# Optimization experiments

Measured on AMD Instinct MI355X. Metric: run time of the kernel, lower is better.

## Reference

```python
import jax, jax.numpy as jnp
import numpy as np
import math

B, L, M = 8, 1024, 1024
H, D, DK, DFF = 16, 1024, 64, 4096
EPS = 1e-5


def _ln(x, g, b):
    mu = jnp.mean(x, axis=-1, keepdims=True)
    var = jnp.mean((x - mu) ** 2, axis=-1, keepdims=True)
    return (x - mu) * jax.lax.rsqrt(var + EPS) * g + b


def _mha(x, kv, Wq, bq, Wk, bk, Wv, bv, Wo, bo, masked):
    # x: [B,Lq,D], kv: [B,Lk,D]; per-head weights stacked: Wq [H,D,DK], bq [H,DK]
    Q = jnp.einsum('bld,hdk->bhlk', x, Wq) + bq[None, :, None, :]
    K = jnp.einsum('bld,hdk->bhlk', kv, Wk) + bk[None, :, None, :]
    V = jnp.einsum('bld,hdk->bhlk', kv, Wv) + bv[None, :, None, :]
    scores = jnp.einsum('bhqk,bhmk->bhqm', Q, K) / math.sqrt(DK)
    p = jax.nn.softmax(scores, axis=-1)
    if masked:
        # faithful to source: mask applied AFTER softmax (multiply by tril ones)
        Lq = x.shape[1]
        tril = jnp.tril(jnp.ones((Lq, kv.shape[1]), dtype=p.dtype))
        p = p * tril
    z = jnp.einsum('bhqm,bhmk->bhqk', p, V)  # [B,H,Lq,DK]
    z = jnp.transpose(z, (0, 2, 1, 3)).reshape(x.shape[0], x.shape[1], H * DK)
    return z @ Wo + bo


def _forward(x, enc, Wq1, bq1, Wk1, bk1, Wv1, bv1, Wo1, bo1,
             Wq2, bq2, Wk2, bk2, Wv2, bv2, Wo2, bo2,
             W1, b1, W2, b2, g1, be1, g2, be2, g3, be3):
    z = _mha(x, x, Wq1, bq1, Wk1, bk1, Wv1, bv1, Wo1, bo1, masked=True)
    x = _ln(z + x, g1, be1)
    z = _mha(x, enc, Wq2, bq2, Wk2, bk2, Wv2, bv2, Wo2, bo2, masked=False)
    x = _ln(z + x, g2, be2)
    # Conv1d(k=1) pair == per-token MLP: relu(x @ W1 + b1) @ W2 + b2
    y = jax.nn.relu(x @ W1 + b1) @ W2 + b2
    return _ln(y + x, g3, be3)


def setup_inputs() -> dict:
    key = jax.random.key(0)
    ks = jax.random.split(key, 16)
    s = 0.02
    return {
        'x': jax.random.normal(ks[0], (B, L, D), jnp.float32),
        'enc': jax.random.normal(ks[1], (B, M, D), jnp.float32),
        'Wq1': jax.random.normal(ks[2], (H, D, DK), jnp.float32) * s,
        'bq1': jnp.zeros((H, DK), jnp.float32),
        'Wk1': jax.random.normal(ks[3], (H, D, DK), jnp.float32) * s,
        'bk1': jnp.zeros((H, DK), jnp.float32),
        'Wv1': jax.random.normal(ks[4], (H, D, DK), jnp.float32) * s,
        'bv1': jnp.zeros((H, DK), jnp.float32),
        'Wo1': jax.random.normal(ks[5], (H * DK, D), jnp.float32) * s,
        'bo1': jnp.zeros((D,), jnp.float32),
        'Wq2': jax.random.normal(ks[6], (H, D, DK), jnp.float32) * s,
        'bq2': jnp.zeros((H, DK), jnp.float32),
        'Wk2': jax.random.normal(ks[7], (H, D, DK), jnp.float32) * s,
        'bk2': jnp.zeros((H, DK), jnp.float32),
        'Wv2': jax.random.normal(ks[8], (H, D, DK), jnp.float32) * s,
        'bv2': jnp.zeros((H, DK), jnp.float32),
        'Wo2': jax.random.normal(ks[9], (H * DK, D), jnp.float32) * s,
        'bo2': jnp.zeros((D,), jnp.float32),
        'W1': jax.random.normal(ks[10], (D, DFF), jnp.float32) * s,
        'b1': jnp.zeros((DFF,), jnp.float32),
        'W2': jax.random.normal(ks[11], (DFF, D), jnp.float32) * s,
        'b2': jnp.zeros((D,), jnp.float32),
        'g1': jnp.ones((D,), jnp.float32), 'be1': jnp.zeros((D,), jnp.float32),
        'g2': jnp.ones((D,), jnp.float32), 'be2': jnp.zeros((D,), jnp.float32),
        'g3': jnp.ones((D,), jnp.float32), 'be3': jnp.zeros((D,), jnp.float32),
    }


def reference(x, enc, Wq1, bq1, Wk1, bk1, Wv1, bv1, Wo1, bo1,
              Wq2, bq2, Wk2, bk2, Wv2, bv2, Wo2, bo2,
              W1, b1, W2, b2, g1, be1, g2, be2, g3, be3):
    return _forward(x, enc, Wq1, bq1, Wk1, bk1, Wv1, bv1, Wo1, bo1,
                    Wq2, bq2, Wk2, bk2, Wv2, bv2, Wo2, bo2,
                    W1, b1, W2, b2, g1, be1, g2, be2, g3, be3)
```

## Files before the change

### kernel.cpp

```cpp
#include <hip/hip_runtime.h>
#include <hip/hip_bf16.h>

typedef __bf16 bf16;
typedef __bf16 bf16x8 __attribute__((ext_vector_type(8)));
typedef __bf16 bf16x4v __attribute__((ext_vector_type(4)));
typedef float f32x4 __attribute__((ext_vector_type(4)));
typedef unsigned int u32;
typedef u32 u32x4 __attribute__((ext_vector_type(4)));

#define DEV static __device__ __forceinline__

DEV void gll16(const void* g, void* l) {
  __builtin_amdgcn_global_load_lds((__attribute__((address_space(1))) void*)g,
                                   (__attribute__((address_space(3))) void*)l,
                                   16, 0, 0);
}

DEV bf16 tobf(float f) { return (bf16)f; }

DEV u32 cvtpk(float lo, float hi) {
  u32 r;
  asm("v_cvt_pk_bf16_f32 %0, %1, %2" : "=v"(r) : "v"(lo), "v"(hi));
  return r;
}

__global__ void cast_f2b_kernel(const float* __restrict__ in, bf16* __restrict__ out, int n4) {
  int i = blockIdx.x * 256 + threadIdx.x;
  if (i < n4) {
    const float4 v = ((const float4*)in)[i];
    bf16x4v o;
    o[0] = tobf(v.x); o[1] = tobf(v.y); o[2] = tobf(v.z); o[3] = tobf(v.w);
    ((bf16x4v*)out)[i] = o;
  }
}

__global__ __launch_bounds__(256)
void tpack_kernel(const float* __restrict__ in, bf16* __restrict__ out,
                  int K, int N, int in_hs, int out_hs, float scale) {
  __shared__ float tile[32][33];
  const int k0 = blockIdx.x << 5, n0 = blockIdx.y << 5;
  const float* ip = in + (size_t)blockIdx.z * in_hs;
  bf16* op = out + (size_t)blockIdx.z * out_hs;
  const int tx = threadIdx.x & 31, ty = threadIdx.x >> 5;
#pragma unroll
  for (int r = 0; r < 4; ++r)
    tile[ty * 4 + r][tx] = ip[(size_t)(k0 + ty * 4 + r) * N + n0 + tx];
  __syncthreads();
#pragma unroll
  for (int r = 0; r < 4; ++r)
    op[(size_t)(n0 + ty * 4 + r) * K + k0 + tx] = tobf(tile[tx][ty * 4 + r] * scale);
}

__global__ void bscale_kernel(const float* __restrict__ in, float* __restrict__ out, int n, float s) {
  int i = blockIdx.x * 256 + threadIdx.x;
  if (i < n) out[i] = in[i] * s;
}

template<int EPI>
__global__ __launch_bounds__(256, 2)
void gemm_bt(const bf16* __restrict__ A, const bf16* __restrict__ W,
             const float* __restrict__ bias, const float* __restrict__ resid,
             void* __restrict__ outv, int M, int N, int K) {
  __shared__ bf16 sA[2][128 * 64];
  __shared__ bf16 sB[2][128 * 64];
  const int nbx = N >> 7;
  const int nwg = (M >> 7) * nbx;
  int bid = (int)blockIdx.x;
  bid = (bid & 7) * (nwg >> 3) + (bid >> 3);
  const int tm = bid / nbx, tn = bid - tm * nbx;
  const int tid = threadIdx.x;
  const int lane = tid & 63;
  const int w = tid >> 6;
  const int wm = (w >> 1) << 6, wn = (w & 1) << 6;
  const int l15 = lane & 15, l4 = lane >> 4;

  int srow[4], scol[4];
#pragma unroll
  for (int j = 0; j < 4; ++j) {
    int g = tid + (j << 8);
    srow[j] = g >> 3;
    scol[j] = ((g & 7) ^ (srow[j] & 7)) << 3;
  }
  const bf16* Abase = A + (size_t)(tm * 128) * K;
  const bf16* Bbase = W + (size_t)(tn * 128) * K;

  f32x4 acc[4][4] = {};
  const int nt = K >> 6;
  int cur = 0;

  auto stage = [&](int buf, int t) {
    const int kb = t << 6;
#pragma unroll
    for (int j = 0; j < 4; ++j) {
      int g = tid + (j << 8);
      gll16(Abase + (size_t)srow[j] * K + kb + scol[j], &sA[buf][g << 3]);
    }
#pragma unroll
    for (int j = 0; j < 4; ++j) {
      int g = tid + (j << 8);
      gll16(Bbase + (size_t)srow[j] * K + kb + scol[j], &sB[buf][g << 3]);
    }
  };

  stage(0, 0);
  __syncthreads();

  for (int t = 0; t < nt; ++t) {
    if (t + 1 < nt) stage(cur ^ 1, t + 1);
    bf16x8 af[4][2], bfm[4][2];
#pragma unroll
    for (int mi = 0; mi < 4; ++mi)
#pragma unroll
      for (int kk = 0; kk < 2; ++kk) {
        int r = wm + (mi << 4) + l15;
        int off = (r << 7) + (kk << 6) + (l4 << 4);
        off ^= (r & 7) << 4;
        af[mi][kk] = *(const bf16x8*)((const char*)sA[cur] + off);
      }
#pragma unroll
    for (int ni = 0; ni < 4; ++ni)
#pragma unroll
      for (int kk = 0; kk < 2; ++kk) {
        int r = wn + (ni << 4) + l15;
        int off = (r << 7) + (kk << 6) + (l4 << 4);
        off ^= (r & 7) << 4;
        bfm[ni][kk] = *(const bf16x8*)((const char*)sB[cur] + off);
      }
#pragma unroll
    for (int mi = 0; mi < 4; ++mi)
#pragma unroll
      for (int ni = 0; ni < 4; ++ni)
#pragma unroll
        for (int kk = 0; kk < 2; ++kk)
          acc[mi][ni] = __builtin_amdgcn_mfma_f32_16x16x32_bf16(af[mi][kk], bfm[ni][kk],
                                                                acc[mi][ni], 0, 0, 0);
    __syncthreads();
    cur ^= 1;
  }

  const int row0 = tm * 128 + wm + (l4 << 2);
  const int col0 = tn * 128 + wn + l15;
#pragma unroll
  for (int ni = 0; ni < 4; ++ni) {
    const int col = col0 + (ni << 4);
    const float bv = bias ? bias[col] : 0.f;
#pragma unroll
    for (int mi = 0; mi < 4; ++mi) {
      const int rr = row0 + (mi << 4);
      f32x4 v = acc[mi][ni];
      if (EPI == 0) {
        bf16* out = (bf16*)outv;
#pragma unroll
        for (int r = 0; r < 4; ++r) out[(size_t)(rr + r) * N + col] = tobf(v[r] + bv);
      } else if (EPI == 1) {
        float* out = (float*)outv;
#pragma unroll
        for (int r = 0; r < 4; ++r) {
          size_t idx = (size_t)(rr + r) * N + col;
          out[idx] = v[r] + bv + resid[idx];
        }
      } else if (EPI == 2) {
        bf16* out = (bf16*)outv;
#pragma unroll
        for (int r = 0; r < 4; ++r) out[(size_t)(rr + r) * N + col] = tobf(fmaxf(v[r] + bv, 0.f));
      } else {
        bf16* out = (bf16*)outv;
        const int bb = rr >> 10, l0 = rr & 1023;
        const int hh = col >> 6, dk = col & 63;
        bf16x4v pk;
#pragma unroll
        for (int r = 0; r < 4; ++r) pk[r] = tobf(v[r] + bv);
        *(bf16x4v*)(out + ((size_t)((bb * 16 + hh) * 64 + dk) << 10) + l0) = pk;
      }
    }
  }
}

template<bool MASKED>
__global__ __launch_bounds__(256, 4)
void attn_kernel(const bf16* __restrict__ Qp, const bf16* __restrict__ Kp,
                 const bf16* __restrict__ Vt, bf16* __restrict__ Z) {
  __shared__ bf16 sK[2][64 * 64];
  __shared__ bf16 sV[2][64 * 64];
  const int Lk = 1024;
  const int d = blockIdx.x;
  const int bh = d & 127, qb = d >> 7;
  const int b = bh >> 4, h = bh & 15;
  const int q0 = qb << 7;
  const int tid = threadIdx.x, lane = tid & 63, w = tid >> 6;
  const int l15 = lane & 15, l4 = lane >> 4;

  const bf16* Qb = Qp + ((size_t)(b * 1024 + q0 + w * 32)) * 1024 + h * 64;
  bf16x8 qf[2][2];
#pragma unroll
  for (int mi = 0; mi < 2; ++mi)
#pragma unroll
    for (int kk = 0; kk < 2; ++kk)
      qf[mi][kk] = *(const bf16x8*)(Qb + (size_t)((mi << 4) + l15) * 1024 + (kk << 5) + (l4 << 3));

  f32x4 o[4][2] = {};
  float Mr[2] = {-1e30f, -1e30f}, Lr[2] = {0.f, 0.f};

  const bf16* Kb = Kp + ((size_t)b * Lk) * 1024 + h * 64;
  const bf16* Vb = Vt + ((size_t)(b * 16 + h)) * 64 * Lk;

  auto stage = [&](int buf, int t, bool withV) {
    const int kv0 = t << 6;
#pragma unroll
    for (int j = 0; j < 2; ++j) {
      int g = tid + (j << 8);
      int r = g >> 3;
      int sc = ((g & 7) ^ (r & 7)) << 3;
      gll16(Kb + (size_t)(kv0 + r) * 1024 + sc, &sK[buf][g << 3]);
      if (withV) gll16(Vb + (size_t)r * Lk + kv0 + sc, &sV[buf][g << 3]);
    }
  };
  auto needPV = [&](int t) -> bool { return !MASKED || ((t << 6) < q0 + 128); };

  const int NT = Lk >> 6;
  stage(0, 0, true);
  __syncthreads();
  int cur = 0;

  for (int t = 0; t < NT; ++t) {
    if (t + 1 < NT) stage(cur ^ 1, t + 1, needPV(t + 1));
    const int kv0 = t << 6;

    f32x4 s[4][2] = {};
#pragma unroll
    for (int n = 0; n < 4; ++n) {
      bf16x8 kf[2];
#pragma unroll
      for (int kk = 0; kk < 2; ++kk) {
        int r = (n << 4) + l15;
        int off = (r << 7) + (kk << 6) + (l4 << 4);
        off ^= (r & 7) << 4;
        kf[kk] = *(const bf16x8*)((const char*)sK[cur] + off);
      }
#pragma unroll
      for (int mi = 0; mi < 2; ++mi)
#pragma unroll
        for (int kk = 0; kk < 2; ++kk)
          s[n][mi] = __builtin_amdgcn_mfma_f32_16x16x32_bf16(kf[kk], qf[mi][kk],
                                                             s[n][mi], 0, 0, 0);
    }

    float alv[2];
#pragma unroll
    for (int mi = 0; mi < 2; ++mi) {
      float tmx = s[0][mi][0];
#pragma unroll
      for (int n = 0; n < 4; ++n)
#pragma unroll
        for (int r = 0; r < 4; ++r) tmx = fmaxf(tmx, s[n][mi][r]);
      tmx = fmaxf(tmx, __shfl_xor(tmx, 16, 64));
      tmx = fmaxf(tmx, __shfl_xor(tmx, 32, 64));
      const float Mn = fmaxf(Mr[mi], tmx);
      alv[mi] = exp2f(Mr[mi] - Mn);
      float rs = 0.f;
#pragma unroll
      for (int n = 0; n < 4; ++n)
#pragma unroll
        for (int r = 0; r < 4; ++r) {
          float p = exp2f(s[n][mi][r] - Mn);
          s[n][mi][r] = p;
          rs += p;
        }
      rs += __shfl_xor(rs, 16, 64);
      rs += __shfl_xor(rs, 32, 64);
      Lr[mi] = Lr[mi] * alv[mi] + rs;
      Mr[mi] = Mn;
    }

#pragma unroll
    for (int mi = 0; mi < 2; ++mi)
#pragma unroll
      for (int r = 0; r < 4; ++r) {
        float a = __shfl(alv[mi], (l4 << 2) + r, 64);
#pragma unroll
        for (int nd = 0; nd < 4; ++nd) o[nd][mi][r] *= a;
      }

    if (needPV(t)) {
      const bool needMask = MASKED && (kv0 + 63 > q0 + (w << 5));
      bf16x8 pa[2][2];
#pragma unroll
      for (int mi = 0; mi < 2; ++mi) {
        u32 D0[4], D1[4];
        const int qg = q0 + (w << 5) + (mi << 4) + l15;
#pragma unroll
        for (int n = 0; n < 4; ++n) {
          float pv[4];
#pragma unroll
          for (int r = 0; r < 4; ++r) {
            float p = s[n][mi][r];
            if (needMask) {
              int cg = kv0 + (n << 4) + (l4 << 2) + r;
              if (cg > qg) p = 0.f;
            }
            pv[r] = p;
          }
          D0[n] = cvtpk(pv[0], pv[1]);
          D1[n] = cvtpk(pv[2], pv[3]);
        }
        const int src = l15 + ((lane & 16) << 1);
#pragma unroll
        for (int kk = 0; kk < 2; ++kk) {
          u32 v0 = (lane & 32) ? D0[2 * kk + 1] : D0[2 * kk];
          u32 v1 = (lane & 32) ? D1[2 * kk + 1] : D1[2 * kk];
          u32x4 tw;
          tw[0] = (u32)__shfl((int)v0, src, 64);
          tw[1] = (u32)__shfl((int)v1, src, 64);
          tw[2] = (u32)__shfl((int)v0, src + 16, 64);
          tw[3] = (u32)__shfl((int)v1, src + 16, 64);
          pa[mi][kk] = *(bf16x8*)&tw;
        }
      }
#pragma unroll
      for (int nd = 0; nd < 4; ++nd) {
        bf16x8 vf[2];
#pragma unroll
        for (int kk = 0; kk < 2; ++kk) {
          int r = (nd << 4) + l15;
          int off = (r << 7) + (kk << 6) + (l4 << 4);
          off ^= (r & 7) << 4;
          vf[kk] = *(const bf16x8*)((const char*)sV[cur] + off);
        }
#pragma unroll
        for (int mi = 0; mi < 2; ++mi)
#pragma unroll
          for (int kk = 0; kk < 2; ++kk)
            o[nd][mi] = __builtin_amdgcn_mfma_f32_16x16x32_bf16(pa[mi][kk], vf[kk],
                                                                o[nd][mi], 0, 0, 0);
      }
    }
    __syncthreads();
    cur ^= 1;
  }

  float inv[2][4];
#pragma unroll
  for (int mi = 0; mi < 2; ++mi) {
    float il = 1.f / Lr[mi];
#pragma unroll
    for (int r = 0; r < 4; ++r) inv[mi][r] = __shfl(il, (l4 << 2) + r, 64);
  }
  bf16* Zb = Z + ((size_t)(b * 1024 + q0 + w * 32)) * 1024 + h * 64;
#pragma unroll
  for (int nd = 0; nd < 4; ++nd)
#pragma unroll
    for (int mi = 0; mi < 2; ++mi)
#pragma unroll
      for (int r = 0; r < 4; ++r)
        Zb[(size_t)((mi << 4) + (l4 << 2) + r) * 1024 + (nd << 4) + l15] =
            tobf(o[nd][mi][r] * inv[mi][r]);
}

__global__ __launch_bounds__(256)
void ln_kernel(const float* __restrict__ in, const float* __restrict__ gw,
               const float* __restrict__ bw, float* __restrict__ outf,
               bf16* __restrict__ outb) {
  const int row = blockIdx.x, tid = threadIdx.x;
  const size_t base = (size_t)row << 10;
  const float4 v = *(const float4*)(in + base + tid * 4);
  float s = v.x + v.y + v.z + v.w;
  float ss = v.x * v.x + v.y * v.y + v.z * v.z + v.w * v.w;
#pragma unroll
  for (int d = 1; d < 64; d <<= 1) { s += __shfl_xor(s, d, 64); ss += __shfl_xor(ss, d, 64); }
  __shared__ float red[8];
  const int w = tid >> 6;
  if ((tid & 63) == 0) { red[w] = s; red[4 + w] = ss; }
  __syncthreads();
  s = red[0] + red[1] + red[2] + red[3];
  ss = red[4] + red[5] + red[6] + red[7];
  const float mu = s * (1.f / 1024.f);
  const float var = ss * (1.f / 1024.f) - mu * mu;
  const float rstd = rsqrtf(var + 1e-5f);
  const float4 g4 = *(const float4*)(gw + tid * 4);
  const float4 b4 = *(const float4*)(bw + tid * 4);
  const float o0 = (v.x - mu) * rstd * g4.x + b4.x;
  const float o1 = (v.y - mu) * rstd * g4.y + b4.y;
  const float o2 = (v.z - mu) * rstd * g4.z + b4.z;
  const float o3 = (v.w - mu) * rstd * g4.w + b4.w;
  if (outf) { float4 of; of.x = o0; of.y = o1; of.z = o2; of.w = o3;
              *(float4*)(outf + base + tid * 4) = of; }
  if (outb) { bf16x4v ob; ob[0] = tobf(o0); ob[1] = tobf(o1); ob[2] = tobf(o2); ob[3] = tobf(o3);
              *(bf16x4v*)(outb + base + tid * 4) = ob; }
}

extern "C" void kernel_launch(void* const* d_in, const int* in_sizes, int n_in,
                              void* d_out, int out_size, void* d_ws, size_t ws_size,
                              hipStream_t stream) {
  const float* x   = (const float*)d_in[0];
  const float* enc = (const float*)d_in[1];
  const float* Wq1 = (const float*)d_in[2];
  const float* bq1 = (const float*)d_in[3];
  const float* Wk1 = (const float*)d_in[4];
  const float* bk1 = (const float*)d_in[5];
  const float* Wv1 = (const float*)d_in[6];
  const float* bv1 = (const float*)d_in[7];
  const float* Wo1 = (const float*)d_in[8];
  const float* bo1 = (const float*)d_in[9];
  const float* Wq2 = (const float*)d_in[10];
  const float* bq2 = (const float*)d_in[11];
  const float* Wk2 = (const float*)d_in[12];
  const float* bk2 = (const float*)d_in[13];
  const float* Wv2 = (const float*)d_in[14];
  const float* bv2 = (const float*)d_in[15];
  const float* Wo2 = (const float*)d_in[16];
  const float* bo2 = (const float*)d_in[17];
  const float* W1  = (const float*)d_in[18];
  const float* b1  = (const float*)d_in[19];
  const float* W2  = (const float*)d_in[20];
  const float* b2  = (const float*)d_in[21];
  const float* g1  = (const float*)d_in[22];
  const float* be1 = (const float*)d_in[23];
  const float* g2  = (const float*)d_in[24];
  const float* be2 = (const float*)d_in[25];
  const float* g3  = (const float*)d_in[26];
  const float* be3 = (const float*)d_in[27];

  char* ws = (char*)d_ws;
  size_t off = 0;
  auto alloc = [&](size_t bytes) { char* p = ws + off; off += (bytes + 255) & ~(size_t)255; return p; };
  const size_t ACT = (size_t)8 * 1024 * 1024 * 2;
  const size_t WSQ = (size_t)1024 * 1024 * 2;
  const float QSC = 0.125f * 1.44269504088896f;

  bf16* xb    = (bf16*)alloc(ACT);
  bf16* encb  = (bf16*)alloc(ACT);
  bf16* Wq1t  = (bf16*)alloc(WSQ);
  bf16* Wk1t  = (bf16*)alloc(WSQ);
  bf16* Wv1t  = (bf16*)alloc(WSQ);
  bf16* Wq2t  = (bf16*)alloc(WSQ);
  bf16* Wk2t  = (bf16*)alloc(WSQ);
  bf16* Wv2t  = (bf16*)alloc(WSQ);
  bf16* Wo1t  = (bf16*)alloc(WSQ);
  bf16* Wo2t  = (bf16*)alloc(WSQ);
  bf16* W1t   = (bf16*)alloc((size_t)4096 * 1024 * 2);
  bf16* W2t   = (bf16*)alloc((size_t)4096 * 1024 * 2);
  float* sbq1 = (float*)alloc(4096);
  float* sbq2 = (float*)alloc(4096);
  char*  S    = alloc((size_t)64 * 1024 * 1024);
  float* rbuf = (float*)alloc((size_t)8 * 1024 * 1024 * 4);
  float* xnf  = (float*)alloc((size_t)8 * 1024 * 1024 * 4);
  bf16*  xnb  = (bf16*)alloc(ACT);

  bf16* q1   = (bf16*)(S);
  bf16* k1   = (bf16*)(S + ACT);
  bf16* vt1  = (bf16*)(S + 2 * ACT);
  bf16* z1   = (bf16*)(S + 3 * ACT);
  bf16* hbuf = (bf16*)S;

  dim3 b256(256);
  cast_f2b_kernel<<<8192, b256, 0, stream>>>(x, xb, 2097152);
  cast_f2b_kernel<<<8192, b256, 0, stream>>>(enc, encb, 2097152);
  tpack_kernel<<<dim3(32, 2, 16), b256, 0, stream>>>(Wq1, Wq1t, 1024, 64, 65536, 65536, QSC);
  tpack_kernel<<<dim3(32, 2, 16), b256, 0, stream>>>(Wk1, Wk1t, 1024, 64, 65536, 65536, 1.f);
  tpack_kernel<<<dim3(32, 2, 16), b256, 0, stream>>>(Wv1, Wv1t, 1024, 64, 65536, 65536, 1.f);
  tpack_kernel<<<dim3(32, 2, 16), b256, 0, stream>>>(Wq2, Wq2t, 1024, 64, 65536, 65536, QSC);
  tpack_kernel<<<dim3(32, 2, 16), b256, 0, stream>>>(Wk2, Wk2t, 1024, 64, 65536, 65536, 1.f);
  tpack_kernel<<<dim3(32, 2, 16), b256, 0, stream>>>(Wv2, Wv2t, 1024, 64, 65536, 65536, 1.f);
  tpack_kernel<<<dim3(32, 32, 1), b256, 0, stream>>>(Wo1, Wo1t, 1024, 1024, 0, 0, 1.f);
  tpack_kernel<<<dim3(32, 32, 1), b256, 0, stream>>>(Wo2, Wo2t, 1024, 1024, 0, 0, 1.f);
  tpack_kernel<<<dim3(32, 128, 1), b256, 0, stream>>>(W1, W1t, 1024, 4096, 0, 0, 1.f);
  tpack_kernel<<<dim3(128, 32, 1), b256, 0, stream>>>(W2, W2t, 4096, 1024, 0, 0, 1.f);
  bscale_kernel<<<4, b256, 0, stream>>>(bq1, sbq1, 1024, QSC);
  bscale_kernel<<<4, b256, 0, stream>>>(bq2, sbq2, 1024, QSC);

  gemm_bt<0><<<512, b256, 0, stream>>>(xb, Wq1t, sbq1, nullptr, q1, 8192, 1024, 1024);
  gemm_bt<0><<<512, b256, 0, stream>>>(xb, Wk1t, bk1, nullptr, k1, 8192, 1024, 1024);
  gemm_bt<3><<<512, b256, 0, stream>>>(xb, Wv1t, bv1, nullptr, vt1, 8192, 1024, 1024);
  attn_kernel<true><<<1024, b256, 0, stream>>>(q1, k1, vt1, z1);
  gemm_bt<1><<<512, b256, 0, stream>>>(z1, Wo1t, bo1, x, rbuf, 8192, 1024, 1024);
  ln_kernel<<<8192, b256, 0, stream>>>(rbuf, g1, be1, xnf, xnb);

  gemm_bt<0><<<512, b256, 0, stream>>>(xnb, Wq2t, sbq2, nullptr, q1, 8192, 1024, 1024);
  gemm_bt<0><<<512, b256, 0, stream>>>(encb, Wk2t, bk2, nullptr, k1, 8192, 1024, 1024);
  gemm_bt<3><<<512, b256, 0, stream>>>(encb, Wv2t, bv2, nullptr, vt1, 8192, 1024, 1024);
  attn_kernel<false><<<1024, b256, 0, stream>>>(q1, k1, vt1, z1);
  gemm_bt<1><<<512, b256, 0, stream>>>(z1, Wo2t, bo2, xnf, rbuf, 8192, 1024, 1024);
  ln_kernel<<<8192, b256, 0, stream>>>(rbuf, g2, be2, xnf, xnb);

  gemm_bt<2><<<2048, b256, 0, stream>>>(xnb, W1t, b1, nullptr, hbuf, 8192, 4096, 1024);
  gemm_bt<1><<<512, b256, 0, stream>>>(hbuf, W2t, b2, xnf, rbuf, 8192, 1024, 4096);
  ln_kernel<<<8192, b256, 0, stream>>>(rbuf, g3, be3, (float*)d_out, nullptr);
}
```

Before: 693.9 us.

## Fuse QKV and KV projection GEMMs into single wide GEMM launches

Packs the Q/K/V weights (and cross-attention K/V weights) into one concatenated weight matrix and runs a single GEMM with N=3072 or 2048 instead of three or two separate launches. A new epilogue routes each column segment to Q/K row-major output or transposed V output. This saves launch overhead and tail effects, and gives each launch more blocks to fill the GPU. It also lowers the attention kernel's occupancy hint from 4 to 3 waves-per-block launch bound, which frees registers at the cost of fewer resident blocks.

```diff
diff --git a/kernel.cpp b/kernel.cpp
--- a/kernel.cpp
+++ b/kernel.cpp
@@ -163,7 +163,7 @@
         bf16* out = (bf16*)outv;
 #pragma unroll
         for (int r = 0; r < 4; ++r) out[(size_t)(rr + r) * N + col] = tobf(fmaxf(v[r] + bv, 0.f));
-      } else {
+      } else if (EPI == 3) {
         bf16* out = (bf16*)outv;
         const int bb = rr >> 10, l0 = rr & 1023;
         const int hh = col >> 6, dk = col & 63;
@@ -171,13 +171,31 @@
 #pragma unroll
         for (int r = 0; r < 4; ++r) pk[r] = tobf(v[r] + bv);
         *(bf16x4v*)(out + ((size_t)((bb * 16 + hh) * 64 + dk) << 10) + l0) = pk;
+      } else {
+        bf16* out = (bf16*)outv;
+        const int seg = tn >> 3;
+        const int cc = col & 1023;
+        const bool isV = (EPI == 4) ? (seg == 2) : (seg == 1);
+        if (isV) {
+          bf16* vout = out + (size_t)seg * 8388608;
+          const int bb = rr >> 10, l0 = rr & 1023;
+          const int hh = cc >> 6, dk = cc & 63;
+          bf16x4v pk;
+#pragma unroll
+          for (int r = 0; r < 4; ++r) pk[r] = tobf(v[r] + bv);
+          *(bf16x4v*)(vout + ((size_t)((bb * 16 + hh) * 64 + dk) << 10) + l0) = pk;
+        } else {
+          bf16* qout = out + (size_t)seg * 8388608;
+#pragma unroll
+          for (int r = 0; r < 4; ++r) qout[(size_t)(rr + r) * 1024 + cc] = tobf(v[r] + bv);
+        }
       }
     }
   }
 }
 
 template<bool MASKED>
-__global__ __launch_bounds__(256, 4)
+__global__ __launch_bounds__(256, 3)
 void attn_kernel(const bf16* __restrict__ Qp, const bf16* __restrict__ Kp,
                  const bf16* __restrict__ Vt, bf16* __restrict__ Z) {
   __shared__ bf16 sK[2][64 * 64];
@@ -424,27 +442,24 @@
   size_t off = 0;
   auto alloc = [&](size_t bytes) { char* p = ws + off; off += (bytes + 255) & ~(size_t)255; return p; };
   const size_t ACT = (size_t)8 * 1024 * 1024 * 2;
-  const size_t WSQ = (size_t)1024 * 1024 * 2;
   const float QSC = 0.125f * 1.44269504088896f;
 
-  bf16* xb    = (bf16*)alloc(ACT);
-  bf16* encb  = (bf16*)alloc(ACT);
-  bf16* Wq1t  = (bf16*)alloc(WSQ);
-  bf16* Wk1t  = (bf16*)alloc(WSQ);
-  bf16* Wv1t  = (bf16*)alloc(WSQ);
-  bf16* Wq2t  = (bf16*)alloc(WSQ);
-  bf16* Wk2t  = (bf16*)alloc(WSQ);
-  bf16* Wv2t  = (bf16*)alloc(WSQ);
-  bf16* Wo1t  = (bf16*)alloc(WSQ);
-  bf16* Wo2t  = (bf16*)alloc(WSQ);
-  bf16* W1t   = (bf16*)alloc((size_t)4096 * 1024 * 2);
-  bf16* W2t   = (bf16*)alloc((size_t)4096 * 1024 * 2);
-  float* sbq1 = (float*)alloc(4096);
-  float* sbq2 = (float*)alloc(4096);
-  char*  S    = alloc((size_t)64 * 1024 * 1024);
-  float* rbuf = (float*)alloc((size_t)8 * 1024 * 1024 * 4);
-  float* xnf  = (float*)alloc((size_t)8 * 1024 * 1024 * 4);
-  bf16*  xnb  = (bf16*)alloc(ACT);
+  bf16* xb     = (bf16*)alloc(ACT);
+  bf16* encb   = (bf16*)alloc(ACT);
+  bf16* Wqkv1t = (bf16*)alloc((size_t)3072 * 1024 * 2);
+  bf16* Wkv2t  = (bf16*)alloc((size_t)2048 * 1024 * 2);
+  bf16* Wq2t   = (bf16*)alloc((size_t)1024 * 1024 * 2);
+  bf16* Wo1t   = (bf16*)alloc((size_t)1024 * 1024 * 2);
+  bf16* Wo2t   = (bf16*)alloc((size_t)1024 * 1024 * 2);
+  bf16* W1t    = (bf16*)alloc((size_t)4096 * 1024 * 2);
+  bf16* W2t    = (bf16*)alloc((size_t)4096 * 1024 * 2);
+  float* qkvb1 = (float*)alloc(3072 * 4);
+  float* kvb2  = (float*)alloc(2048 * 4);
+  float* sbq2  = (float*)alloc(1024 * 4);
+  char*  S     = alloc((size_t)64 * 1024 * 1024);
+  float* rbuf  = (float*)alloc((size_t)8 * 1024 * 1024 * 4);
+  float* xnf   = (float*)alloc((size_t)8 * 1024 * 1024 * 4);
+  bf16*  xnb   = (bf16*)alloc(ACT);
 
   bf16* q1   = (bf16*)(S);
   bf16* k1   = (bf16*)(S + ACT);
@@ -455,29 +470,30 @@
   dim3 b256(256);
   cast_f2b_kernel<<<8192, b256, 0, stream>>>(x, xb, 2097152);
   cast_f2b_kernel<<<8192, b256, 0, stream>>>(enc, encb, 2097152);
-  tpack_kernel<<<dim3(32, 2, 16), b256, 0, stream>>>(Wq1, Wq1t, 1024, 64, 65536, 65536, QSC);
-  tpack_kernel<<<dim3(32, 2, 16), b256, 0, stream>>>(Wk1, Wk1t, 1024, 64, 65536, 65536, 1.f);
-  tpack_kernel<<<dim3(32, 2, 16), b256, 0, stream>>>(Wv1, Wv1t, 1024, 64, 65536, 65536, 1.f);
+  tpack_kernel<<<dim3(32, 2, 16), b256, 0, stream>>>(Wq1, Wqkv1t, 1024, 64, 65536, 65536, QSC);
+  tpack_kernel<<<dim3(32, 2, 16), b256, 0, stream>>>(Wk1, Wqkv1t + 1048576, 1024, 64, 65536, 65536, 1.f);
+  tpack_kernel<<<dim3(32, 2, 16), b256, 0, stream>>>(Wv1, Wqkv1t + 2097152, 1024, 64, 65536, 65536, 1.f);
   tpack_kernel<<<dim3(32, 2, 16), b256, 0, stream>>>(Wq2, Wq2t, 1024, 64, 65536, 65536, QSC);
-  tpack_kernel<<<dim3(32, 2, 16), b256, 0, stream>>>(Wk2, Wk2t, 1024, 64, 65536, 65536, 1.f);
-  tpack_kernel<<<dim3(32, 2, 16), b256, 0, stream>>>(Wv2, Wv2t, 1024, 64, 65536, 65536, 1.f);
+  tpack_kernel<<<dim3(32, 2, 16), b256, 0, stream>>>(Wk2, Wkv2t, 1024, 64, 65536, 65536, 1.f);
+  tpack_kernel<<<dim3(32, 2, 16), b256, 0, stream>>>(Wv2, Wkv2t + 1048576, 1024, 64, 65536, 65536, 1.f);
   tpack_kernel<<<dim3(32, 32, 1), b256, 0, stream>>>(Wo1, Wo1t, 1024, 1024, 0, 0, 1.f);
   tpack_kernel<<<dim3(32, 32, 1), b256, 0, stream>>>(Wo2, Wo2t, 1024, 1024, 0, 0, 1.f);
   tpack_kernel<<<dim3(32, 128, 1), b256, 0, stream>>>(W1, W1t, 1024, 4096, 0, 0, 1.f);
   tpack_kernel<<<dim3(128, 32, 1), b256, 0, stream>>>(W2, W2t, 4096, 1024, 0, 0, 1.f);
-  bscale_kernel<<<4, b256, 0, stream>>>(bq1, sbq1, 1024, QSC);
+  bscale_kernel<<<4, b256, 0, stream>>>(bq1, qkvb1, 1024, QSC);
+  bscale_kernel<<<4, b256, 0, stream>>>(bk1, qkvb1 + 1024, 1024, 1.f);
+  bscale_kernel<<<4, b256, 0, stream>>>(bv1, qkvb1 + 2048, 1024, 1.f);
+  bscale_kernel<<<4, b256, 0, stream>>>(bk2, kvb2, 1024, 1.f);
+  bscale_kernel<<<4, b256, 0, stream>>>(bv2, kvb2 + 1024, 1024, 1.f);
   bscale_kernel<<<4, b256, 0, stream>>>(bq2, sbq2, 1024, QSC);
 
-  gemm_bt<0><<<512, b256, 0, stream>>>(xb, Wq1t, sbq1, nullptr, q1, 8192, 1024, 1024);
-  gemm_bt<0><<<512, b256, 0, stream>>>(xb, Wk1t, bk1, nullptr, k1, 8192, 1024, 1024);
-  gemm_bt<3><<<512, b256, 0, stream>>>(xb, Wv1t, bv1, nullptr, vt1, 8192, 1024, 1024);
+  gemm_bt<4><<<1536, b256, 0, stream>>>(xb, Wqkv1t, qkvb1, nullptr, q1, 8192, 3072, 1024);
   attn_kernel<true><<<1024, b256, 0, stream>>>(q1, k1, vt1, z1);
   gemm_bt<1><<<512, b256, 0, stream>>>(z1, Wo1t, bo1, x, rbuf, 8192, 1024, 1024);
   ln_kernel<<<8192, b256, 0, stream>>>(rbuf, g1, be1, xnf, xnb);
 
   gemm_bt<0><<<512, b256, 0, stream>>>(xnb, Wq2t, sbq2, nullptr, q1, 8192, 1024, 1024);
-  gemm_bt<0><<<512, b256, 0, stream>>>(encb, Wk2t, bk2, nullptr, k1, 8192, 1024, 1024);
-  gemm_bt<3><<<512, b256, 0, stream>>>(encb, Wv2t, bv2, nullptr, vt1, 8192, 1024, 1024);
+  gemm_bt<5><<<1024, b256, 0, stream>>>(encb, Wkv2t, kvb2, nullptr, k1, 8192, 2048, 1024);
   attn_kernel<false><<<1024, b256, 0, stream>>>(q1, k1, vt1, z1);
   gemm_bt<1><<<512, b256, 0, stream>>>(z1, Wo2t, bo2, xnf, rbuf, 8192, 1024, 1024);
   ln_kernel<<<8192, b256, 0, stream>>>(rbuf, g2, be2, xnf, xnb);
```

After: 645.3 us. 1.08x faster.
